# Kernel optimization log

Measured on AMD Instinct MI355X. Metric: run time of the kernel, lower is better.

The kernel has to match this reference:

```python
import jax, jax.numpy as jnp
import numpy as np

N_NODES = 100000
D_IN = 128
H_DIM = 128
N_EDGES = 1600000


def _gcn_conv(x, src, dst, dinv, W, b):
    # PyG GCNConv(improved=True): h = x @ W; out = A_hat h + b,
    # A_hat = D^{-1/2} (A + 2I) D^{-1/2}
    h = x @ W                                   # [N, H]
    norm = dinv[src] * dinv[dst]                # [E]
    agg = jnp.zeros_like(h).at[dst].add(h[src] * norm[:, None])
    agg = agg + h * (2.0 * dinv * dinv)[:, None]  # self-loop, weight 2.0
    return agg + b


def setup_inputs() -> dict:
    key = jax.random.key(0)
    ks = jax.random.split(key, 12)
    s = 1.0 / np.sqrt(D_IN)
    sh = 1.0 / np.sqrt(2 * H_DIM)
    inp = {
        "x": jax.random.normal(ks[0], (N_NODES, D_IN), jnp.float32),
        "edge_index": jax.random.randint(ks[1], (2, N_EDGES), 0, N_NODES, jnp.int64),
        # GCNConv weights (in -> hidden), bias
        "Wz": jax.random.uniform(ks[2], (D_IN, H_DIM), jnp.float32, -s, s),
        "bz": jnp.zeros((H_DIM,), jnp.float32),
        "Wr": jax.random.uniform(ks[3], (D_IN, H_DIM), jnp.float32, -s, s),
        "br": jnp.zeros((H_DIM,), jnp.float32),
        "Wh": jax.random.uniform(ks[4], (D_IN, H_DIM), jnp.float32, -s, s),
        "bh": jnp.zeros((H_DIM,), jnp.float32),
        # TGCN gate linears: Linear(2h, h)
        "lzW": jax.random.uniform(ks[5], (2 * H_DIM, H_DIM), jnp.float32, -sh, sh),
        "lzb": jax.random.uniform(ks[6], (H_DIM,), jnp.float32, -sh, sh),
        "lrW": jax.random.uniform(ks[7], (2 * H_DIM, H_DIM), jnp.float32, -sh, sh),
        "lrb": jax.random.uniform(ks[8], (H_DIM,), jnp.float32, -sh, sh),
        "lhW": jax.random.uniform(ks[9], (2 * H_DIM, H_DIM), jnp.float32, -sh, sh),
        "lhb": jax.random.uniform(ks[10], (H_DIM,), jnp.float32, -sh, sh),
        # final linear2: hidden -> 1
        "W2": jax.random.uniform(ks[11], (H_DIM, 1), jnp.float32, -1 / np.sqrt(H_DIM), 1 / np.sqrt(H_DIM)),
        "b2": jnp.zeros((1,), jnp.float32),
    }
    return inp


def reference(x, edge_index, Wz, bz, Wr, br, Wh, bh, lzW, lzb, lrW, lrb, lhW, lhb, W2, b2):
    src, dst = edge_index[0], edge_index[1]
    n = x.shape[0]
    # improved GCN norm: deg includes self-loop weight 2
    deg = jnp.zeros((n,), x.dtype).at[dst].add(jnp.ones_like(src, x.dtype)) + 2.0
    dinv = jnp.where(deg > 0, deg ** -0.5, 0.0)
    # TGCN cell with H0 = 0
    H0 = jnp.zeros((n, Wz.shape[1]), x.dtype)
    Z = jax.nn.sigmoid(jnp.concatenate([_gcn_conv(x, src, dst, dinv, Wz, bz), H0], axis=1) @ lzW + lzb)
    R = jax.nn.sigmoid(jnp.concatenate([_gcn_conv(x, src, dst, dinv, Wr, br), H0], axis=1) @ lrW + lrb)
    Ht = jnp.tanh(jnp.concatenate([_gcn_conv(x, src, dst, dinv, Wh, bh), H0 * R], axis=1) @ lhW + lhb)
    H = Z * H0 + (1.0 - Z) * Ht
    # forward: relu output is discarded (y = h overwrites), then linear2
    return H @ W2 + b2
```

## Files before the change

kernel.cpp:

```cpp
#include <hip/hip_runtime.h>
#include <math.h>

#define D 128
#define BSHIFT 9
#define NB 196
#define EPT 7
#define P1B 241
#define CAPB 80
#define PSTRIDE (P1B * CAPB)
#define ECAP 9216
#define P2B NB
#define XCB2 3125
#define PRB 32

typedef __attribute__((ext_vector_type(8))) short s8v;
typedef __attribute__((ext_vector_type(8))) unsigned short us8;
typedef __attribute__((ext_vector_type(4))) unsigned short us4;
typedef __attribute__((ext_vector_type(4))) float f4v;

__device__ __forceinline__ float bf2f(unsigned short u) {
    union { unsigned int i; float f; } v; v.i = ((unsigned int)u) << 16; return v.f;
}
__device__ __forceinline__ unsigned short f2bf(float f) {
    union { float f; unsigned int i; } v; v.f = f;
    unsigned int r = v.i + 0x7FFFu + ((v.i >> 16) & 1u);
    return (unsigned short)(r >> 16);
}

__global__ __launch_bounds__(1024) void k_part1(
    const int* __restrict__ src, const int* __restrict__ dst, int E,
    unsigned int* __restrict__ pairs, int* __restrict__ runlen) {
    __shared__ int cnt[256];
    __shared__ int loff[256];
    __shared__ int ts[256];
    __shared__ unsigned int stage[EPT * 1024];
    int bx = blockIdx.x, tid = threadIdx.x;

    unsigned int pk[EPT]; int rkbk[EPT];
    int e0 = bx * (EPT * 1024) + tid;
    if (tid < 256) cnt[tid] = 0;
    __syncthreads();
    #pragma unroll
    for (int i = 0; i < EPT; ++i) {
        int e = e0 + i * 1024;
        bool ok = e < E;
        int d = ok ? dst[e] : 0;
        int s = ok ? src[e] : 0;
        int bk = d >> BSHIFT;
        pk[i] = ((unsigned int)(d & ((1 << BSHIFT) - 1)) << 17) | (unsigned int)s;
        int r = ok ? atomicAdd(&cnt[bk], 1) : 0;
        rkbk[i] = ok ? ((bk << 16) | r) : -1;
    }
    __syncthreads();
    if (tid < 256) ts[tid] = cnt[tid];
    __syncthreads();
    for (int off = 1; off < 256; off <<= 1) {
        int add = 0;
        if (tid < 256 && tid >= off) add = ts[tid - off];
        __syncthreads();
        if (tid < 256) ts[tid] += add;
        __syncthreads();
    }
    if (tid < 256) loff[tid] = ts[tid] - cnt[tid];
    __syncthreads();
    #pragma unroll
    for (int i = 0; i < EPT; ++i) {
        if (rkbk[i] >= 0) {
            int bk = rkbk[i] >> 16;
            stage[loff[bk] + (rkbk[i] & 0xffff)] = pk[i];
        }
    }
    if (tid < 256) runlen[bx * 256 + tid] = cnt[tid];
    __syncthreads();
    int wv = tid >> 6, lane = tid & 63;
    for (int b = wv; b < 256; b += 16) {
        int len = cnt[b];
        if (len == 0) continue;
        int lo = loff[b];
        unsigned int gbase = (unsigned int)b * PSTRIDE + (unsigned int)bx * CAPB;
        for (int j = lane; j < len; j += 64)
            pairs[gbase + j] = stage[lo + j];
    }
}

__global__ __launch_bounds__(1024) void k_mid(
    const unsigned int* __restrict__ pairs, const int* __restrict__ runlen,
    int N,
    int* __restrict__ rowptr, int* __restrict__ deg, float* __restrict__ dinv,
    int* __restrict__ esrc,
    const float* __restrict__ x, unsigned short* __restrict__ xb, int n4,
    const float* __restrict__ Wz, const float* __restrict__ bz,
    const float* __restrict__ lzW, const float* __restrict__ lzb,
    const float* __restrict__ Wh, const float* __restrict__ bh,
    const float* __restrict__ lhW, const float* __restrict__ lhb,
    unsigned short* __restrict__ Mt, float* __restrict__ c) {
    int bx = blockIdx.x, tid = threadIdx.x;

    if (bx < P2B) {
        __shared__ int cnt2[512];
        __shared__ int lcur[512];
        __shared__ int ts[256];
        __shared__ int rl[256];
        int b = bx;
        int n0 = b << BSHIFT;
        int nn = min(N - n0, 1 << BSHIFT);
        long pb = (long)b * PSTRIDE;
        int wv = tid >> 6, lane = tid & 63;

        if (tid < 256) rl[tid] = (tid < P1B) ? runlen[tid * 256 + b] : 0;
        if (tid < 512) cnt2[tid] = 0;
        __syncthreads();
        for (int r = wv; r < P1B; r += 16) {
            int len = rl[r];
            long rb = pb + r * CAPB;
            for (int j = lane; j < len; j += 64)
                atomicAdd(&cnt2[pairs[rb + j] >> 17], 1);
        }
        __syncthreads();
        int a0 = 0, a1 = 0, s = 0;
        if (tid < 256) {
            a0 = cnt2[2 * tid]; a1 = cnt2[2 * tid + 1];
            s = a0 + a1;
            ts[tid] = s;
        }
        __syncthreads();
        for (int off = 1; off < 256; off <<= 1) {
            int add = 0;
            if (tid < 256 && tid >= off) add = ts[tid - off];
            __syncthreads();
            if (tid < 256) ts[tid] += add;
            __syncthreads();
        }
        if (tid < 256) {
            int excl = ts[tid] - s;
            int base0 = b * ECAP + excl;
            lcur[2 * tid]     = base0;
            lcur[2 * tid + 1] = base0 + a0;
            if (2 * tid < nn) {
                rowptr[n0 + 2 * tid] = base0;
                deg[n0 + 2 * tid]    = a0;
                dinv[n0 + 2 * tid]   = rsqrtf((float)a0 + 2.0f);
            }
            if (2 * tid + 1 < nn) {
                rowptr[n0 + 2 * tid + 1] = base0 + a0;
                deg[n0 + 2 * tid + 1]    = a1;
                dinv[n0 + 2 * tid + 1]   = rsqrtf((float)a1 + 2.0f);
            }
        }
        __syncthreads();
        for (int r = wv; r < P1B; r += 16) {
            int len = rl[r];
            long rb = pb + r * CAPB;
            for (int j = lane; j < len; j += 64) {
                unsigned int p = pairs[rb + j];
                int dl = p >> 17;
                int pos = atomicAdd(&lcur[dl], 1);
                esrc[pos] = (int)(p & 0x1FFFFu);
            }
        }
    } else if (bx < P2B + XCB2) {
        int i = (bx - P2B) * 1024 + tid;
        if (i < n4) {
            float4 v = ((const float4*)x)[i];
            us4 o;
            o[0] = f2bf(v.x); o[1] = f2bf(v.y); o[2] = f2bf(v.z); o[3] = f2bf(v.w);
            ((us4*)xb)[i] = o;
        }
    } else {
        int k = (bx - (P2B + XCB2)) * 4 + (tid >> 8);
        int j = tid & 255;
        int jj = j & 127;
        const float* W = (j < 128) ? Wz : Wh;
        const float* L = (j < 128) ? lzW : lhW;
        float s = 0.f;
        for (int t = 0; t < 128; ++t) s += W[k * 128 + t] * L[t * 128 + jj];
        Mt[(size_t)j * 128 + k] = f2bf(s);
        if (k == 0) {
            const float* b  = (j < 128) ? bz  : bh;
            const float* lb = (j < 128) ? lzb : lhb;
            float cs = lb[jj];
            for (int t = 0; t < 128; ++t) cs += b[t] * L[t * 128 + jj];
            c[j] = cs;
        }
    }
}

__global__ __launch_bounds__(256) void k_gather(const unsigned short* __restrict__ xb,
                                                const int* __restrict__ esrc,
                                                const int* __restrict__ rowptr,
                                                const int* __restrict__ deg,
                                                const float* __restrict__ dinv,
                                                unsigned short* __restrict__ xab, int N) {
    int node = (blockIdx.x * blockDim.x + threadIdx.x) >> 5;
    int sub  = threadIdx.x & 31;
    if (node >= N) return;
    int eo = sub >> 4, cs = sub & 15;
    int start = rowptr[node];
    int end = start + deg[node];
    float dd = dinv[node];
    float acc[8];
    #pragma unroll
    for (int j = 0; j < 8; ++j) acc[j] = 0.f;

    for (int base = start; base < end; base += 32) {
        int cnt = min(32, end - base);
        int myedge = 0; float mynorm = 0.f;
        if (sub < cnt) { myedge = esrc[base + sub]; mynorm = dinv[myedge]; }
        int pairs = (cnt + 1) >> 1;
        int i = 0;
        for (; i + 3 < pairs; i += 4) {
            int i0 = 2 * i + eo;
            int   s0 = __shfl(myedge, i0,     32); float w0 = __shfl(mynorm, i0,     32);
            int   s1 = __shfl(myedge, i0 + 2, 32); float w1 = __shfl(mynorm, i0 + 2, 32);
            int   s2 = __shfl(myedge, i0 + 4, 32); float w2 = __shfl(mynorm, i0 + 4, 32);
            int   s3 = __shfl(myedge, i0 + 6, 32); float w3 = __shfl(mynorm, i0 + 6, 32);
            us8 v0 = *(const us8*)(xb + (size_t)s0 * D + cs * 8);
            us8 v1 = *(const us8*)(xb + (size_t)s1 * D + cs * 8);
            us8 v2 = *(const us8*)(xb + (size_t)s2 * D + cs * 8);
            us8 v3 = *(const us8*)(xb + (size_t)s3 * D + cs * 8);
            #pragma unroll
            for (int j = 0; j < 8; ++j) acc[j] += bf2f(v0[j]) * w0;
            #pragma unroll
            for (int j = 0; j < 8; ++j) acc[j] += bf2f(v1[j]) * w1;
            #pragma unroll
            for (int j = 0; j < 8; ++j) acc[j] += bf2f(v2[j]) * w2;
            #pragma unroll
            for (int j = 0; j < 8; ++j) acc[j] += bf2f(v3[j]) * w3;
        }
        for (; i < pairs; ++i) {
            int i0 = 2 * i + eo;
            int   s0 = __shfl(myedge, i0, 32); float w0 = __shfl(mynorm, i0, 32);
            us8 v0 = *(const us8*)(xb + (size_t)s0 * D + cs * 8);
            #pragma unroll
            for (int j = 0; j < 8; ++j) acc[j] += bf2f(v0[j]) * w0;
        }
    }
    #pragma unroll
    for (int j = 0; j < 8; ++j) acc[j] += __shfl_xor(acc[j], 16);
    if (eo == 0) {
        us8 xs = *(const us8*)(xb + (size_t)node * D + cs * 8);
        float sfac = 2.f * dd * dd;
        us8 r;
        #pragma unroll
        for (int j = 0; j < 8; ++j) r[j] = f2bf(acc[j] * dd + bf2f(xs[j]) * sfac);
        *(us8*)(xab + (size_t)node * D + cs * 8) = r;
    }
}

#define ASTRIDE 136
__global__ __launch_bounds__(256, 4) void k_ep_mfma(
    const unsigned short* __restrict__ xab, const unsigned short* __restrict__ Mt,
    const float* __restrict__ c, const float* __restrict__ W2,
    const float* __restrict__ b2, float* __restrict__ out, int N) {
    __shared__ unsigned short Ast[64 * ASTRIDE];
    __shared__ float pbuf[4][64];

    int tid = threadIdx.x;
    int n0 = blockIdx.x * 64;
    int wv = tid >> 6;
    int lane = tid & 63;
    int l = lane & 15, q = lane >> 4;

    #pragma unroll
    for (int j = 0; j < 4; ++j) {
        int idx = tid + 256 * j;
        int row = idx >> 4, c16 = idx & 15;
        us8 v = {0, 0, 0, 0, 0, 0, 0, 0};
        if (n0 + row < N) v = *(const us8*)(xab + (size_t)(n0 + row) * D + c16 * 8);
        *(us8*)&Ast[row * ASTRIDE + c16 * 8] = v;
    }
    __syncthreads();

    int tz0 = 2 * wv;
    f4v acc[4][4];
    #pragma unroll
    for (int i = 0; i < 4; ++i)
        #pragma unroll
        for (int nt = 0; nt < 4; ++nt) acc[i][nt] = (f4v){0.f, 0.f, 0.f, 0.f};

    const unsigned short* Bb = Mt + (size_t)l * 128 + q * 8;

    #pragma unroll
    for (int ks = 0; ks < 4; ++ks) {
        s8v b[4];
        #pragma unroll
        for (int i = 0; i < 2; ++i) {
            b[i]     = *(const s8v*)(Bb + (size_t)(tz0 + i) * 16 * 128 + ks * 32);
            b[2 + i] = *(const s8v*)(Bb + (size_t)(8 + tz0 + i) * 16 * 128 + ks * 32);
        }
        #pragma unroll
        for (int nt = 0; nt < 4; ++nt) {
            s8v a = *(const s8v*)&Ast[(nt * 16 + l) * ASTRIDE + ks * 32 + q * 8];
            #pragma unroll
            for (int i = 0; i < 4; ++i)
                acc[i][nt] = __builtin_amdgcn_mfma_f32_16x16x32_bf16(a, b[i], acc[i][nt], 0, 0, 0);
        }
    }

    float p[4][4];
    #pragma unroll
    for (int nt = 0; nt < 4; ++nt)
        #pragma unroll
        for (int r = 0; r < 4; ++r) p[nt][r] = 0.f;
    #pragma unroll
    for (int i = 0; i < 2; ++i) {
        int col = (tz0 + i) * 16 + l;
        float cz = c[col], ch = c[128 + col], w2 = W2[col];
        #pragma unroll
        for (int nt = 0; nt < 4; ++nt)
            #pragma unroll
            for (int r = 0; r < 4; ++r) {
                float gz = acc[i][nt][r] + cz;
                float gh = acc[2 + i][nt][r] + ch;
                float z  = 1.f / (1.f + __expf(-gz));
                float ht = 1.f - 2.f / (__expf(2.f * gh) + 1.f);
                p[nt][r] += (1.f - z) * ht * w2;
            }
    }
    #pragma unroll
    for (int nt = 0; nt < 4; ++nt)
        #pragma unroll
        for (int r = 0; r < 4; ++r) {
            p[nt][r] += __shfl_xor(p[nt][r], 1);
            p[nt][r] += __shfl_xor(p[nt][r], 2);
            p[nt][r] += __shfl_xor(p[nt][r], 4);
            p[nt][r] += __shfl_xor(p[nt][r], 8);
        }
    if (l == 0) {
        #pragma unroll
        for (int nt = 0; nt < 4; ++nt)
            #pragma unroll
            for (int r = 0; r < 4; ++r)
                pbuf[wv][nt * 16 + q * 4 + r] = p[nt][r];
    }
    __syncthreads();
    if (tid < 64) {
        int n = n0 + tid;
        if (n < N)
            out[n] = pbuf[0][tid] + pbuf[1][tid] + pbuf[2][tid] + pbuf[3][tid] + b2[0];
    }
}

extern "C" void kernel_launch(void* const* d_in, const int* in_sizes, int n_in,
                              void* d_out, int out_size, void* d_ws, size_t ws_size,
                              hipStream_t stream) {
    const float* x    = (const float*)d_in[0];
    const int*   eidx = (const int*)d_in[1];
    const float* Wz   = (const float*)d_in[2];
    const float* bz   = (const float*)d_in[3];
    const float* Wh   = (const float*)d_in[6];
    const float* bh   = (const float*)d_in[7];
    const float* lzW  = (const float*)d_in[8];
    const float* lzb  = (const float*)d_in[9];
    const float* lhW  = (const float*)d_in[12];
    const float* lhb  = (const float*)d_in[13];
    const float* W2   = (const float*)d_in[14];
    const float* b2   = (const float*)d_in[15];
    float* out = (float*)d_out;

    int N = in_sizes[0] / D;
    int E = in_sizes[1] / 2;
    const int* src = eidx;
    const int* dst = eidx + E;

    char* ws = (char*)d_ws;
    size_t off = 0;
    auto alloc = [&](size_t bytes) { void* p = ws + off; off += (bytes + 511) & ~(size_t)511; return p; };
    unsigned short* xb  = (unsigned short*)alloc((size_t)N * D * 2);
    unsigned short* xab = (unsigned short*)alloc((size_t)N * D * 2);
    int*   rowptr = (int*)  alloc((size_t)N * 4);
    int*   deg    = (int*)  alloc((size_t)N * 4);
    float* dinv   = (float*)alloc((size_t)N * 4);
    int*   esrc   = (int*)  alloc((size_t)NB * ECAP * 4);
    int*   runlen = (int*)  alloc((size_t)P1B * 256 * 4);
    unsigned short* Mt = (unsigned short*)alloc(256 * 128 * 2);
    float* c      = (float*)alloc(256 * 4);
    unsigned int* pairs = (unsigned int*)xab;

    int n4 = N * (D / 4);
    k_part1<<<P1B, 1024, 0, stream>>>(src, dst, E, pairs, runlen);
    k_mid<<<P2B + XCB2 + PRB, 1024, 0, stream>>>(
        pairs, runlen, N, rowptr, deg, dinv, esrc,
        x, xb, n4, Wz, bz, lzW, lzb, Wh, bh, lhW, lhb, Mt, c);
    k_gather<<<(N * 32 + 255) / 256, 256, 0, stream>>>(xb, esrc, rowptr, deg, dinv, xab, N);
    k_ep_mfma<<<(N + 63) / 64, 256, 0, stream>>>(xab, Mt, c, W2, b2, out, N);
}
```

Measured before the change: 236.4 us.

## Compact bucket partition with global atomic cursors and overlap with x conversion

The first edge-partition pass now claims contiguous space in each destination bucket through a global atomic cursor, so pairs land packed per bucket rather than in fixed per-block slots indexed by a runlen table. This pass is merged into the same launch as the x-to-bf16 conversion and weight-precompute blocks, so it overlaps with that work. The second pass becomes a separate kernel that loads each bucket's pairs into registers once and reuses them for both counting and scatter, instead of reading them twice from scattered runs. In exchange it adds a memset launch and global atomics, and the edge order inside each node becomes nondeterministic.

```diff
diff --git a/kernel.cpp b/kernel.cpp
--- a/kernel.cpp
+++ b/kernel.cpp
@@ -6,12 +6,10 @@
 #define NB 196
 #define EPT 7
 #define P1B 241
-#define CAPB 80
-#define PSTRIDE (P1B * CAPB)
 #define ECAP 9216
-#define P2B NB
 #define XCB2 3125
 #define PRB 32
+#define PK_PT 9
 
 typedef __attribute__((ext_vector_type(8))) short s8v;
 typedef __attribute__((ext_vector_type(8))) unsigned short us8;
@@ -27,67 +25,9 @@
     return (unsigned short)(r >> 16);
 }
 
-__global__ __launch_bounds__(1024) void k_part1(
+__global__ __launch_bounds__(1024) void k_front(
     const int* __restrict__ src, const int* __restrict__ dst, int E,
-    unsigned int* __restrict__ pairs, int* __restrict__ runlen) {
-    __shared__ int cnt[256];
-    __shared__ int loff[256];
-    __shared__ int ts[256];
-    __shared__ unsigned int stage[EPT * 1024];
-    int bx = blockIdx.x, tid = threadIdx.x;
-
-    unsigned int pk[EPT]; int rkbk[EPT];
-    int e0 = bx * (EPT * 1024) + tid;
-    if (tid < 256) cnt[tid] = 0;
-    __syncthreads();
-    #pragma unroll
-    for (int i = 0; i < EPT; ++i) {
-        int e = e0 + i * 1024;
-        bool ok = e < E;
-        int d = ok ? dst[e] : 0;
-        int s = ok ? src[e] : 0;
-        int bk = d >> BSHIFT;
-        pk[i] = ((unsigned int)(d & ((1 << BSHIFT) - 1)) << 17) | (unsigned int)s;
-        int r = ok ? atomicAdd(&cnt[bk], 1) : 0;
-        rkbk[i] = ok ? ((bk << 16) | r) : -1;
-    }
-    __syncthreads();
-    if (tid < 256) ts[tid] = cnt[tid];
-    __syncthreads();
-    for (int off = 1; off < 256; off <<= 1) {
-        int add = 0;
-        if (tid < 256 && tid >= off) add = ts[tid - off];
-        __syncthreads();
-        if (tid < 256) ts[tid] += add;
-        __syncthreads();
-    }
-    if (tid < 256) loff[tid] = ts[tid] - cnt[tid];
-    __syncthreads();
-    #pragma unroll
-    for (int i = 0; i < EPT; ++i) {
-        if (rkbk[i] >= 0) {
-            int bk = rkbk[i] >> 16;
-            stage[loff[bk] + (rkbk[i] & 0xffff)] = pk[i];
-        }
-    }
-    if (tid < 256) runlen[bx * 256 + tid] = cnt[tid];
-    __syncthreads();
-    int wv = tid >> 6, lane = tid & 63;
-    for (int b = wv; b < 256; b += 16) {
-        int len = cnt[b];
-        if (len == 0) continue;
-        int lo = loff[b];
-        unsigned int gbase = (unsigned int)b * PSTRIDE + (unsigned int)bx * CAPB;
-        for (int j = lane; j < len; j += 64)
-            pairs[gbase + j] = stage[lo + j];
-    }
-}
-
-__global__ __launch_bounds__(1024) void k_mid(
-    const unsigned int* __restrict__ pairs, const int* __restrict__ runlen,
-    int N,
-    int* __restrict__ rowptr, int* __restrict__ deg, float* __restrict__ dinv,
-    int* __restrict__ esrc,
+    int* __restrict__ bcur, unsigned int* __restrict__ pairs,
     const float* __restrict__ x, unsigned short* __restrict__ xb, int n4,
     const float* __restrict__ Wz, const float* __restrict__ bz,
     const float* __restrict__ lzW, const float* __restrict__ lzb,
@@ -96,33 +36,30 @@
     unsigned short* __restrict__ Mt, float* __restrict__ c) {
     int bx = blockIdx.x, tid = threadIdx.x;
 
-    if (bx < P2B) {
-        __shared__ int cnt2[512];
-        __shared__ int lcur[512];
+    if (bx < P1B) {
+        __shared__ int cnt[256];
+        __shared__ int loff[256];
         __shared__ int ts[256];
-        __shared__ int rl[256];
-        int b = bx;
-        int n0 = b << BSHIFT;
-        int nn = min(N - n0, 1 << BSHIFT);
-        long pb = (long)b * PSTRIDE;
-        int wv = tid >> 6, lane = tid & 63;
-
-        if (tid < 256) rl[tid] = (tid < P1B) ? runlen[tid * 256 + b] : 0;
-        if (tid < 512) cnt2[tid] = 0;
-        __syncthreads();
-        for (int r = wv; r < P1B; r += 16) {
-            int len = rl[r];
-            long rb = pb + r * CAPB;
-            for (int j = lane; j < len; j += 64)
-                atomicAdd(&cnt2[pairs[rb + j] >> 17], 1);
-        }
-        __syncthreads();
-        int a0 = 0, a1 = 0, s = 0;
-        if (tid < 256) {
-            a0 = cnt2[2 * tid]; a1 = cnt2[2 * tid + 1];
-            s = a0 + a1;
-            ts[tid] = s;
-        }
+        __shared__ int base[256];
+        __shared__ unsigned int stage[EPT * 1024];
+
+        unsigned int pk[EPT]; int rkbk[EPT];
+        int e0 = bx * (EPT * 1024) + tid;
+        if (tid < 256) cnt[tid] = 0;
+        __syncthreads();
+        #pragma unroll
+        for (int i = 0; i < EPT; ++i) {
+            int e = e0 + i * 1024;
+            bool ok = e < E;
+            int d = ok ? dst[e] : 0;
+            int s = ok ? src[e] : 0;
+            int bk = d >> BSHIFT;
+            pk[i] = ((unsigned int)(d & ((1 << BSHIFT) - 1)) << 17) | (unsigned int)s;
+            int r = ok ? atomicAdd(&cnt[bk], 1) : 0;
+            rkbk[i] = ok ? ((bk << 16) | r) : -1;
+        }
+        __syncthreads();
+        if (tid < 256) ts[tid] = cnt[tid];
         __syncthreads();
         for (int off = 1; off < 256; off <<= 1) {
             int add = 0;
@@ -131,35 +68,29 @@
             if (tid < 256) ts[tid] += add;
             __syncthreads();
         }
-        if (tid < 256) {
-            int excl = ts[tid] - s;
-            int base0 = b * ECAP + excl;
-            lcur[2 * tid]     = base0;
-            lcur[2 * tid + 1] = base0 + a0;
-            if (2 * tid < nn) {
-                rowptr[n0 + 2 * tid] = base0;
-                deg[n0 + 2 * tid]    = a0;
-                dinv[n0 + 2 * tid]   = rsqrtf((float)a0 + 2.0f);
+        if (tid < 256) loff[tid] = ts[tid] - cnt[tid];
+        __syncthreads();
+        #pragma unroll
+        for (int i = 0; i < EPT; ++i) {
+            if (rkbk[i] >= 0) {
+                int bk = rkbk[i] >> 16;
+                stage[loff[bk] + (rkbk[i] & 0xffff)] = pk[i];
             }
-            if (2 * tid + 1 < nn) {
-                rowptr[n0 + 2 * tid + 1] = base0 + a0;
-                deg[n0 + 2 * tid + 1]    = a1;
-                dinv[n0 + 2 * tid + 1]   = rsqrtf((float)a1 + 2.0f);
-            }
-        }
-        __syncthreads();
-        for (int r = wv; r < P1B; r += 16) {
-            int len = rl[r];
-            long rb = pb + r * CAPB;
-            for (int j = lane; j < len; j += 64) {
-                unsigned int p = pairs[rb + j];
-                int dl = p >> 17;
-                int pos = atomicAdd(&lcur[dl], 1);
-                esrc[pos] = (int)(p & 0x1FFFFu);
-            }
-        }
-    } else if (bx < P2B + XCB2) {
-        int i = (bx - P2B) * 1024 + tid;
+        }
+        if (tid < 256 && cnt[tid] > 0)
+            base[tid] = atomicAdd(&bcur[tid], cnt[tid]);
+        __syncthreads();
+        int wv = tid >> 6, lane = tid & 63;
+        for (int b = wv; b < NB; b += 16) {
+            int len = cnt[b];
+            if (len == 0) continue;
+            int lo = loff[b];
+            unsigned int gbase = (unsigned int)b * ECAP + (unsigned int)base[b];
+            for (int j = lane; j < len; j += 64)
+                pairs[gbase + j] = stage[lo + j];
+        }
+    } else if (bx < P1B + XCB2) {
+        int i = (bx - P1B) * 1024 + tid;
         if (i < n4) {
             float4 v = ((const float4*)x)[i];
             us4 o;
@@ -167,7 +98,7 @@
             ((us4*)xb)[i] = o;
         }
     } else {
-        int k = (bx - (P2B + XCB2)) * 4 + (tid >> 8);
+        int k = (bx - (P1B + XCB2)) * 4 + (tid >> 8);
         int j = tid & 255;
         int jj = j & 127;
         const float* W = (j < 128) ? Wz : Wh;
@@ -181,6 +112,75 @@
             float cs = lb[jj];
             for (int t = 0; t < 128; ++t) cs += b[t] * L[t * 128 + jj];
             c[j] = cs;
+        }
+    }
+}
+
+__global__ __launch_bounds__(1024) void k_part2(
+    const unsigned int* __restrict__ pairs, const int* __restrict__ bcur, int N,
+    int* __restrict__ rowptr, int* __restrict__ deg, float* __restrict__ dinv,
+    int* __restrict__ esrc) {
+    __shared__ int cnt2[512];
+    __shared__ int lcur[512];
+    __shared__ int ts[256];
+    int b = blockIdx.x, tid = threadIdx.x;
+    int n0 = b << BSHIFT;
+    int nn = min(N - n0, 1 << BSHIFT);
+    int tot = bcur[b];
+    long pb = (long)b * ECAP;
+
+    unsigned int pk[PK_PT];
+    #pragma unroll
+    for (int k = 0; k < PK_PT; ++k) {
+        int idx = tid + k * 1024;
+        pk[k] = (idx < tot) ? pairs[pb + idx] : 0u;
+    }
+    if (tid < 512) cnt2[tid] = 0;
+    __syncthreads();
+    #pragma unroll
+    for (int k = 0; k < PK_PT; ++k) {
+        int idx = tid + k * 1024;
+        if (idx < tot) atomicAdd(&cnt2[pk[k] >> 17], 1);
+    }
+    __syncthreads();
+    int a0 = 0, a1 = 0, s = 0;
+    if (tid < 256) {
+        a0 = cnt2[2 * tid]; a1 = cnt2[2 * tid + 1];
+        s = a0 + a1;
+        ts[tid] = s;
+    }
+    __syncthreads();
+    for (int off = 1; off < 256; off <<= 1) {
+        int add = 0;
+        if (tid < 256 && tid >= off) add = ts[tid - off];
+        __syncthreads();
+        if (tid < 256) ts[tid] += add;
+        __syncthreads();
+    }
+    if (tid < 256) {
+        int excl = ts[tid] - s;
+        int base0 = b * ECAP + excl;
+        lcur[2 * tid]     = base0;
+        lcur[2 * tid + 1] = base0 + a0;
+        if (2 * tid < nn) {
+            rowptr[n0 + 2 * tid] = base0;
+            deg[n0 + 2 * tid]    = a0;
+            dinv[n0 + 2 * tid]   = rsqrtf((float)a0 + 2.0f);
+        }
+        if (2 * tid + 1 < nn) {
+            rowptr[n0 + 2 * tid + 1] = base0 + a0;
+            deg[n0 + 2 * tid + 1]    = a1;
+            dinv[n0 + 2 * tid + 1]   = rsqrtf((float)a1 + 2.0f);
+        }
+    }
+    __syncthreads();
+    #pragma unroll
+    for (int k = 0; k < PK_PT; ++k) {
+        int idx = tid + k * 1024;
+        if (idx < tot) {
+            int dl = pk[k] >> 17;
+            int pos = atomicAdd(&lcur[dl], 1);
+            esrc[pos] = (int)(pk[k] & 0x1FFFFu);
         }
     }
 }
@@ -372,16 +372,18 @@
     int*   deg    = (int*)  alloc((size_t)N * 4);
     float* dinv   = (float*)alloc((size_t)N * 4);
     int*   esrc   = (int*)  alloc((size_t)NB * ECAP * 4);
-    int*   runlen = (int*)  alloc((size_t)P1B * 256 * 4);
+    int*   bcur   = (int*)  alloc(256 * 4);
     unsigned short* Mt = (unsigned short*)alloc(256 * 128 * 2);
     float* c      = (float*)alloc(256 * 4);
     unsigned int* pairs = (unsigned int*)xab;
 
+    hipMemsetAsync(bcur, 0, 256 * sizeof(int), stream);
+
     int n4 = N * (D / 4);
-    k_part1<<<P1B, 1024, 0, stream>>>(src, dst, E, pairs, runlen);
-    k_mid<<<P2B + XCB2 + PRB, 1024, 0, stream>>>(
-        pairs, runlen, N, rowptr, deg, dinv, esrc,
-        x, xb, n4, Wz, bz, lzW, lzb, Wh, bh, lhW, lhb, Mt, c);
+    k_front<<<P1B + XCB2 + PRB, 1024, 0, stream>>>(
+        src, dst, E, bcur, pairs, x, xb, n4,
+        Wz, bz, lzW, lzb, Wh, bh, lhW, lhb, Mt, c);
+    k_part2<<<NB, 1024, 0, stream>>>(pairs, bcur, N, rowptr, deg, dinv, esrc);
     k_gather<<<(N * 32 + 255) / 256, 256, 0, stream>>>(xb, esrc, rowptr, deg, dinv, xab, N);
     k_ep_mfma<<<(N + 63) / 64, 256, 0, stream>>>(xab, Mt, c, W2, b2, out, N);
 }
```

New measurement: 241.1 us. No clear change (+2.0%).
